# Optimization experiments

Hardware: AMD Instinct MI355X
Metric: run time of the kernel (lower is better)

Reference implementation:

```python
import jax, jax.numpy as jnp
import numpy as np

# --- MLA config (matches init_kwargs) ---
DIM = 2048
H = 16
KV_RANK = 512
Q_RANK = 1536
ROPE = 64          # qk_rope_head_dim (even)
NOPE = 128         # qk_nope_head_dim
VD = 128           # v_head_dim
THETA = 500000.0
EPS = 1e-6
B, T = 1, 2048
QK_HEAD = NOPE + ROPE  # logits use nope + rope dims


def _rmsnorm(x, w):
    # x float32; RMS over last dim, no mean subtraction
    rms = jax.lax.rsqrt(jnp.mean(x * x, axis=-1, keepdims=True) + EPS)
    return (x * rms) * w


def _rope_tables(t):
    inv_freq = 1.0 / (THETA ** (jnp.arange(0, ROPE, 2, dtype=jnp.float32) / ROPE))  # (ROPE/2,)
    pos = jnp.arange(t, dtype=jnp.float32)
    angles = jnp.outer(pos, inv_freq)  # (T, ROPE/2)
    return jnp.cos(angles), jnp.sin(angles)


def _apply_rope(x, cos, sin):
    # x: (B, T, Hx, D) with adjacent-pair rotation; cos/sin: (T, D/2)
    b, t, h, d = x.shape
    xp = x.reshape(b, t, h, d // 2, 2)
    even, odd = xp[..., 0], xp[..., 1]
    c = cos.reshape(1, t, 1, d // 2)
    s = sin.reshape(1, t, 1, d // 2)
    out = jnp.stack((even * c - odd * s, odd * c + even * s), axis=-1)
    return out.reshape(b, t, h, d)


def setup_inputs() -> dict:
    key = jax.random.key(0)
    ks = jax.random.split(key, 7)
    s = 0.02
    x = jax.random.normal(ks[0], (B, T, DIM), dtype=jnp.float32)
    w_q_down = jax.random.normal(ks[1], (Q_RANK, DIM), dtype=jnp.float32) * s
    q_norm_w = jnp.ones((Q_RANK,), dtype=jnp.float32)
    w_q_up = jax.random.normal(ks[2], (H * (NOPE + ROPE), Q_RANK), dtype=jnp.float32) * s
    w_kv_down = jax.random.normal(ks[3], (KV_RANK + ROPE, DIM), dtype=jnp.float32) * s
    kv_norm_w = jnp.ones((KV_RANK,), dtype=jnp.float32)
    w_kv_up = jax.random.normal(ks[4], (H * (NOPE + VD), KV_RANK), dtype=jnp.float32) * s
    w_o = jax.random.normal(ks[5], (DIM, H * VD), dtype=jnp.float32) * s
    return {"x": x, "w_q_down": w_q_down, "q_norm_w": q_norm_w, "w_q_up": w_q_up,
            "w_kv_down": w_kv_down, "kv_norm_w": kv_norm_w, "w_kv_up": w_kv_up, "w_o": w_o}


def reference(x, w_q_down, q_norm_w, w_q_up, w_kv_down, kv_norm_w, w_kv_up, w_o):
    b, t, _ = x.shape
    # Query path: down-proj -> RMSNorm -> up-proj, split nope/rope
    c_q = _rmsnorm(x @ w_q_down.T, q_norm_w)                       # (B,T,Q_RANK)
    q = (c_q @ w_q_up.T).reshape(b, t, H, NOPE + ROPE)
    q_nope, q_rope = q[..., :NOPE], q[..., NOPE:]
    # KV path: down-proj -> split latent c_kv and shared rope key
    kv = x @ w_kv_down.T                                           # (B,T,KV_RANK+ROPE)
    c_kv = kv[..., :KV_RANK]
    k_rope_raw = kv[..., KV_RANK:].reshape(b, t, 1, ROPE)
    # RoPE (adjacent-pair), start_pos=0
    cos, sin = _rope_tables(t)
    q_rope = _apply_rope(q_rope, cos, sin)
    k_rope = _apply_rope(k_rope_raw, cos, sin)                     # (B,T,1,ROPE) shared head
    # Reconstruct k_nope and v from normalized latent
    kv_up = (_rmsnorm(c_kv, kv_norm_w) @ w_kv_up.T).reshape(b, t, H, NOPE + VD)
    k_nope, v = kv_up[..., :NOPE], kv_up[..., NOPE:]
    # Assemble full q/k (rope key broadcast across heads)
    q_full = jnp.concatenate((q_nope, q_rope), axis=-1)            # (B,T,H,QK_HEAD)
    k_full = jnp.concatenate((k_nope, jnp.broadcast_to(k_rope, (b, t, H, ROPE))), axis=-1)
    # Causal attention
    scale = 1.0 / np.sqrt(QK_HEAD)
    scores = jnp.einsum('bqhd,bkhd->bhqk', q_full, k_full) * scale  # (B,H,T,T)
    causal = jnp.tril(jnp.ones((t, t), dtype=bool))
    scores = jnp.where(causal[None, None], scores, -jnp.inf)
    attn = jax.nn.softmax(scores, axis=-1)
    out = jnp.einsum('bhqk,bkhd->bqhd', attn, v).reshape(b, t, H * VD)
    return out @ w_o.T                                             # (B,T,DIM)
```

## Files before the change

kernel.cpp:

```cpp
#include <hip/hip_runtime.h>
#include <hip/hip_bf16.h>

typedef short short8 __attribute__((ext_vector_type(8)));
typedef float f32x4 __attribute__((ext_vector_type(4)));

#define DIM 2048
#define NH 16
#define KV_RANK 512
#define Q_RANK 1536
#define ROPE_D 64
#define NOPE 128
#define VD 128
#define TT 2048
#define QKH 192
#define QD (NH * QKH)
#define KVUP_D (NH * (NOPE + VD))
#define WDN 2176

__device__ inline unsigned short f2bf(float f) {
  __hip_bfloat16 h = __float2bfloat16(f);
  union { __hip_bfloat16 h; unsigned short u; } cv; cv.h = h; return cv.u;
}
__device__ inline float bf2f(unsigned short u) {
  union { unsigned int i; float f; } cv; cv.i = ((unsigned int)u) << 16; return cv.f;
}
__device__ inline void gload_lds16(const void* g, void* l) {
  __builtin_amdgcn_global_load_lds(
      (const __attribute__((address_space(1))) void*)g,
      (__attribute__((address_space(3))) void*)l, 16, 0, 0);
}

__global__ __launch_bounds__(256) void convert_all(
    const float* __restrict__ x, const float* __restrict__ wqd,
    const float* __restrict__ wkvd, const float* __restrict__ wqu,
    const float* __restrict__ wkvu, const float* __restrict__ wo,
    unsigned short* __restrict__ xb, unsigned short* __restrict__ wdb,
    unsigned short* __restrict__ wqub, unsigned short* __restrict__ wkvub,
    unsigned short* __restrict__ wob) {
  int i = blockIdx.x * 256 + threadIdx.x;
  const int n0 = TT * DIM / 4;
  const int n1 = WDN * 2048 / 4;
  const int n2 = QD * Q_RANK / 4;
  const int n3 = KVUP_D * KV_RANK / 4;
  const int n4 = DIM * DIM / 4;
  float4 v;
  unsigned short* dst;
  if (i < n0) { v = reinterpret_cast<const float4*>(x)[i]; dst = xb; }
  else if ((i -= n0) < n1) {
    int row = i >> 9, c4 = i & 511;
    if (row < 1536)      v = reinterpret_cast<const float4*>(wqd)[row * 512 + c4];
    else if (row < 2112) v = reinterpret_cast<const float4*>(wkvd)[(row - 1536) * 512 + c4];
    else                 v = make_float4(0.f, 0.f, 0.f, 0.f);
    dst = wdb;
  }
  else if ((i -= n1) < n2) { v = reinterpret_cast<const float4*>(wqu)[i]; dst = wqub; }
  else if ((i -= n2) < n3) { v = reinterpret_cast<const float4*>(wkvu)[i]; dst = wkvub; }
  else if ((i -= n3) < n4) { v = reinterpret_cast<const float4*>(wo)[i]; dst = wob; }
  else return;
  ushort4 o;
  o.x = f2bf(v.x); o.y = f2bf(v.y); o.z = f2bf(v.z); o.w = f2bf(v.w);
  reinterpret_cast<ushort4*>(dst)[i] = o;
}

__device__ __forceinline__ void gemm_core(const unsigned short* __restrict__ A,
                                          const unsigned short* __restrict__ W,
                                          unsigned short* As, unsigned short* Bs,
                                          int K, int lda, int ldb,
                                          int bm, int bn, int tid,
                                          f32x4 (&acc)[4][4]) {
  const int lane = tid & 63, wave = tid >> 6;
  const int wm = (wave >> 1) * 64, wn = (wave & 1) * 64;
  const int fr = lane & 15, fg = lane >> 4;
  const int sr = lane >> 3, scb = (lane & 7) ^ sr;
  const int r0 = wave * 32;

  const unsigned short* Ag = A + (size_t)(bm + r0 + sr) * lda + scb * 8;
  const unsigned short* Wg = W + (size_t)(bn + r0 + sr) * ldb + scb * 8;
  const int nt = K >> 6;

#pragma unroll
  for (int i = 0; i < 4; ++i) {
    gload_lds16(Ag + (size_t)(i * 8) * lda, As + r0 * 64 + i * 512);
    gload_lds16(Wg + (size_t)(i * 8) * ldb, Bs + r0 * 64 + i * 512);
  }
  int cur = 0;
  for (int t = 0; t < nt; ++t) {
    if (t + 1 < nt) {
      const int nb = cur ^ 1;
      const int ko = (t + 1) * 64;
#pragma unroll
      for (int i = 0; i < 4; ++i) {
        gload_lds16(Ag + ko + (size_t)(i * 8) * lda, As + nb * 8192 + r0 * 64 + i * 512);
        gload_lds16(Wg + ko + (size_t)(i * 8) * ldb, Bs + nb * 8192 + r0 * 64 + i * 512);
      }
      asm volatile("s_waitcnt vmcnt(8)" ::: "memory");
    } else {
      asm volatile("s_waitcnt vmcnt(0)" ::: "memory");
    }
    __builtin_amdgcn_s_barrier();
    asm volatile("" ::: "memory");
    const unsigned short* Ac = As + cur * 8192;
    const unsigned short* Bc = Bs + cur * 8192;
    __builtin_amdgcn_s_setprio(1);
#pragma unroll
    for (int kk = 0; kk < 2; ++kk) {
      short8 a[4], b[4];
#pragma unroll
      for (int i = 0; i < 4; ++i) {
        int ra = wm + i * 16 + fr;
        a[i] = *reinterpret_cast<const short8*>(&Ac[ra * 64 + (((kk * 4 + fg) ^ (ra & 7)) * 8)]);
        int rb = wn + i * 16 + fr;
        b[i] = *reinterpret_cast<const short8*>(&Bc[rb * 64 + (((kk * 4 + fg) ^ (rb & 7)) * 8)]);
      }
#pragma unroll
      for (int i = 0; i < 4; ++i)
#pragma unroll
        for (int j = 0; j < 4; ++j)
          acc[i][j] = __builtin_amdgcn_mfma_f32_16x16x32_bf16(a[i], b[j], acc[i][j], 0, 0, 0);
    }
    __builtin_amdgcn_s_setprio(0);
    asm volatile("" ::: "memory");
    __builtin_amdgcn_s_barrier();
    cur ^= 1;
  }
}

__device__ __forceinline__ void gemm_core_sb(const unsigned short* __restrict__ A,
                                             const unsigned short* __restrict__ W,
                                             unsigned short* As, unsigned short* Bs,
                                             int K, int lda, int ldb,
                                             int bm, int bn, int tid,
                                             f32x4 (&acc)[4][4]) {
  const int lane = tid & 63, wave = tid >> 6;
  const int wm = (wave >> 1) * 64, wn = (wave & 1) * 64;
  const int fr = lane & 15, fg = lane >> 4;
  const int sr = lane >> 3, scb = (lane & 7) ^ sr;
  const int r0 = wave * 32;

  const unsigned short* Ag = A + (size_t)(bm + r0 + sr) * lda + scb * 8;
  const unsigned short* Wg = W + (size_t)(bn + r0 + sr) * ldb + scb * 8;

  for (int k0 = 0; k0 < K; k0 += 64) {
#pragma unroll
    for (int i = 0; i < 4; ++i) {
      gload_lds16(Ag + k0 + (size_t)(i * 8) * lda, As + r0 * 64 + i * 512);
      gload_lds16(Wg + k0 + (size_t)(i * 8) * ldb, Bs + r0 * 64 + i * 512);
    }
    __syncthreads();
    __builtin_amdgcn_s_setprio(1);
#pragma unroll
    for (int kk = 0; kk < 2; ++kk) {
      short8 a[4], b[4];
#pragma unroll
      for (int i = 0; i < 4; ++i) {
        int ra = wm + i * 16 + fr;
        a[i] = *reinterpret_cast<const short8*>(&As[ra * 64 + (((kk * 4 + fg) ^ (ra & 7)) * 8)]);
        int rb = wn + i * 16 + fr;
        b[i] = *reinterpret_cast<const short8*>(&Bs[rb * 64 + (((kk * 4 + fg) ^ (rb & 7)) * 8)]);
      }
#pragma unroll
      for (int i = 0; i < 4; ++i)
#pragma unroll
        for (int j = 0; j < 4; ++j)
          acc[i][j] = __builtin_amdgcn_mfma_f32_16x16x32_bf16(a[i], b[j], acc[i][j], 0, 0, 0);
    }
    __builtin_amdgcn_s_setprio(0);
    __syncthreads();
  }
}

__global__ __launch_bounds__(256) void gemm_fast(const unsigned short* __restrict__ A,
                                                 const unsigned short* __restrict__ W,
                                                 float* __restrict__ Cf,
                                                 unsigned short* __restrict__ Cb,
                                                 int K, int lda, int ldb, int ldc) {
  __shared__ __align__(16) unsigned short As[2 * 128 * 64];
  __shared__ __align__(16) unsigned short Bs[2 * 128 * 64];
  const int tid = threadIdx.x;
  const int bm = blockIdx.y * 128, bn = blockIdx.x * 128;
  const int lane = tid & 63, wave = tid >> 6;
  const int wm = (wave >> 1) * 64, wn = (wave & 1) * 64;
  const int fr = lane & 15, fg = lane >> 4;

  f32x4 acc[4][4] = {};
  gemm_core(A, W, As, Bs, K, lda, ldb, bm, bn, tid, acc);

  if (Cb) {
#pragma unroll
    for (int i = 0; i < 4; ++i) {
      int row0 = bm + wm + i * 16 + fg * 4;
#pragma unroll
      for (int j = 0; j < 4; ++j) {
        int col = bn + wn + j * 16 + fr;
#pragma unroll
        for (int r = 0; r < 4; ++r)
          Cb[(size_t)(row0 + r) * ldc + col] = f2bf(acc[i][j][r]);
      }
    }
  } else {
#pragma unroll
    for (int i = 0; i < 4; ++i) {
      int row0 = bm + wm + i * 16 + fg * 4;
#pragma unroll
      for (int j = 0; j < 4; ++j) {
        int col = bn + wn + j * 16 + fr;
#pragma unroll
        for (int r = 0; r < 4; ++r)
          Cf[(size_t)(row0 + r) * ldc + col] = acc[i][j][r];
      }
    }
  }
}

__global__ __launch_bounds__(256) void gemm_dual(
    const unsigned short* __restrict__ A1, const unsigned short* __restrict__ W1,
    unsigned short* __restrict__ C1,
    const unsigned short* __restrict__ A2, const unsigned short* __restrict__ W2,
    unsigned short* __restrict__ kbuf, unsigned short* __restrict__ vt) {
  __shared__ __align__(16) unsigned short As[128 * 64];
  __shared__ __align__(16) unsigned short Bs[128 * 64];
  const int tid = threadIdx.x;
  const int s = blockIdx.x;
  const unsigned short *A, *W;
  int K, lda, bm, bn;
  const bool isq = (s < 384);
  if (isq) {
    A = A1; W = W1; K = Q_RANK; lda = Q_RANK;
    bn = (s % 24) * 128; bm = (s / 24) * 128;
  } else {
    int b2 = s - 384;
    A = A2; W = W2; K = KV_RANK; lda = KV_RANK;
    bn = (b2 & 31) * 128; bm = (b2 >> 5) * 128;
  }
  const int lane = tid & 63, wave = tid >> 6;
  const int wm = (wave >> 1) * 64, wn = (wave & 1) * 64;
  const int fr = lane & 15, fg = lane >> 4;

  f32x4 acc[4][4] = {};
  gemm_core_sb(A, W, As, Bs, K, lda, lda, bm, bn, tid, acc);

  if (isq) {
#pragma unroll
    for (int i = 0; i < 4; ++i) {
      int row0 = bm + wm + i * 16 + fg * 4;
#pragma unroll
      for (int j = 0; j < 4; ++j) {
        int col = bn + wn + j * 16 + fr;
#pragma unroll
        for (int r = 0; r < 4; ++r)
          C1[(size_t)(row0 + r) * QD + col] = f2bf(acc[i][j][r]);
      }
    }
  } else {
#pragma unroll
    for (int i = 0; i < 4; ++i) {
      int row0 = bm + wm + i * 16 + fg * 4;
#pragma unroll
      for (int j = 0; j < 4; ++j) {
        int col = bn + wn + j * 16 + fr;
        int hh = col >> 8, cc = col & 255;
        if (cc < 128) {
#pragma unroll
          for (int r = 0; r < 4; ++r)
            kbuf[((size_t)hh * TT + row0 + r) * QKH + cc] = f2bf(acc[i][j][r]);
        } else {
          ushort4 w4;
          w4.x = f2bf(acc[i][j][0]); w4.y = f2bf(acc[i][j][1]);
          w4.z = f2bf(acc[i][j][2]); w4.w = f2bf(acc[i][j][3]);
          *reinterpret_cast<ushort4*>(vt + (size_t)(hh * VD + cc - 128) * TT + row0) = w4;
        }
      }
    }
  }
}

__global__ __launch_bounds__(256) void rmsnorm_both(
    const unsigned short* __restrict__ cqkv,
    const float* __restrict__ qw, const float* __restrict__ kvw,
    unsigned short* __restrict__ cq, unsigned short* __restrict__ ckv) {
  const int row = blockIdx.x, tid = threadIdx.x;
  __shared__ float red[256];
  const unsigned short* base = cqkv + (size_t)row * WDN;

#pragma unroll
  for (int ph = 0; ph < 2; ++ph) {
    const int cols = ph ? KV_RANK : Q_RANK;
    const int nch = cols >> 3;
    const unsigned short* x = base + (ph ? Q_RANK : 0);
    const float* w = ph ? kvw : qw;
    unsigned short* out = (ph ? ckv : cq) + (size_t)row * cols;
    float ss = 0.f;
    for (int cb = tid; cb < nch; cb += 256) {
      short8 v = *reinterpret_cast<const short8*>(x + cb * 8);
#pragma unroll
      for (int e = 0; e < 8; ++e) { float f = bf2f((unsigned short)v[e]); ss += f * f; }
    }
    red[tid] = ss; __syncthreads();
    for (int off = 128; off > 0; off >>= 1) {
      if (tid < off) red[tid] += red[tid + off];
      __syncthreads();
    }
    float r = rsqrtf(red[0] / (float)cols + 1e-6f);
    __syncthreads();
    for (int cb = tid; cb < nch; cb += 256) {
      short8 v = *reinterpret_cast<const short8*>(x + cb * 8);
      ushort4 o0, o1;
      o0.x = f2bf(bf2f((unsigned short)v[0]) * r * w[cb * 8 + 0]);
      o0.y = f2bf(bf2f((unsigned short)v[1]) * r * w[cb * 8 + 1]);
      o0.z = f2bf(bf2f((unsigned short)v[2]) * r * w[cb * 8 + 2]);
      o0.w = f2bf(bf2f((unsigned short)v[3]) * r * w[cb * 8 + 3]);
      o1.x = f2bf(bf2f((unsigned short)v[4]) * r * w[cb * 8 + 4]);
      o1.y = f2bf(bf2f((unsigned short)v[5]) * r * w[cb * 8 + 5]);
      o1.z = f2bf(bf2f((unsigned short)v[6]) * r * w[cb * 8 + 6]);
      o1.w = f2bf(bf2f((unsigned short)v[7]) * r * w[cb * 8 + 7]);
      *reinterpret_cast<ushort4*>(out + cb * 8) = o0;
      *reinterpret_cast<ushort4*>(out + cb * 8 + 4) = o1;
    }
  }
}

__global__ __launch_bounds__(256) void rope_kernel(unsigned short* __restrict__ qb,
                                                   const unsigned short* __restrict__ cqkv,
                                                   unsigned short* __restrict__ kbuf) {
  const int t = blockIdx.x, tid = threadIdx.x;
  unsigned short* qrow = qb + (size_t)t * QD;
  for (int p = tid; p < NH * 32 + 32; p += 256) {
    int j = (p < NH * 32) ? (p & 31) : (p - NH * 32);
    float inv = powf(500000.0f, -(float)(2 * j) * (1.0f / 64.0f));
    float ang = (float)t * inv;
    float sv, cv;
    sincosf(ang, &sv, &cv);
    if (p < NH * 32) {
      int h = p >> 5;
      unsigned short* b = qrow + h * QKH + NOPE + 2 * j;
      float e = bf2f(b[0]), o = bf2f(b[1]);
      b[0] = f2bf(e * cv - o * sv);
      b[1] = f2bf(o * cv + e * sv);
    } else {
      const unsigned short* b = cqkv + (size_t)t * WDN + 2048 + 2 * j;
      float e = bf2f(b[0]), o = bf2f(b[1]);
      unsigned short re = f2bf(e * cv - o * sv);
      unsigned short ro = f2bf(o * cv + e * sv);
#pragma unroll
      for (int hh = 0; hh < NH; ++hh) {
        kbuf[((size_t)hh * TT + t) * QKH + NOPE + 2 * j]     = re;
        kbuf[((size_t)hh * TT + t) * QKH + NOPE + 2 * j + 1] = ro;
      }
    }
  }
}

__global__ __launch_bounds__(256, 2) void attn_part(
    const unsigned short* __restrict__ qb,
    const unsigned short* __restrict__ kbuf,
    const unsigned short* __restrict__ vtb,
    unsigned short* __restrict__ Opart,
    float* __restrict__ ml)
{
  const int b = blockIdx.x;
  const int h = b & 15;
  const int w = b >> 4;
  int qt, c;
  if (w < 16)      { qt = 15 - (w >> 2); c = w & 3; }
  else if (w < 28) { int v = w - 16; qt = 11 - v / 3; c = v % 3; }
  else if (w < 36) { qt = 7 - ((w - 28) >> 1); c = (w - 28) & 1; }
  else             { qt = 3 - (w - 36); c = 0; }
  const int t0 = qt * 128;
  const int ktlo = c * 8;
  const int kthi = min(c * 8 + 8, 2 * qt + 2);
  const int tid = threadIdx.x;
  const int lane = tid & 63, wv = tid >> 6;
  const int fr = lane & 15, fg = lane >> 4;

  __shared__ __align__(16) unsigned short KVl[2560 * 8];
  __shared__ __align__(16) unsigned short Ps[4][2][16 * 64];
  unsigned short* Kl = KVl;
  unsigned short* Vt = KVl + 12288;

  short8 qf[2][6];
#pragma unroll
  for (int s = 0; s < 2; ++s) {
    const unsigned short* qrow = qb + (size_t)(t0 + wv * 32 + s * 16 + fr) * QD + h * QKH;
#pragma unroll
    for (int kc = 0; kc < 6; ++kc)
      qf[s][kc] = *reinterpret_cast<const short8*>(qrow + kc * 32 + fg * 8);
  }

  f32x4 o[2][8] = {};
  float m2[2] = {-1e30f, -1e30f};
  float l2[2] = {0.f, 0.f};
  const float scale = 0.0721687836487032f;
  const unsigned short* kb = kbuf + (size_t)h * TT * QKH;
  const unsigned short* vb = vtb + (size_t)h * VD * TT;

  for (int kt = ktlo; kt < kthi; ++kt) {
    const int kt0 = kt * 64;
#pragma unroll
    for (int i = 0; i < 6; ++i) {
      int u = tid + i * 256;
      int row = u / 24, cb = u - (u / 24) * 24;
      int cbs = cb ^ (row & 7);
      gload_lds16(kb + (size_t)(kt0 + row) * QKH + cbs * 8, Kl + u * 8);
    }
#pragma unroll
    for (int i = 0; i < 4; ++i) {
      int u = tid + i * 256;
      int d = u >> 3, cb = u & 7;
      int cbs = cb ^ (d & 7);
      gload_lds16(vb + (size_t)d * TT + kt0 + cbs * 8, Vt + u * 8);
    }
    asm volatile("s_waitcnt vmcnt(0)" ::: "memory");
    __syncthreads();

    f32x4 sA[2][4] = {};
    __builtin_amdgcn_s_setprio(1);
#pragma unroll
    for (int kc = 0; kc < 6; ++kc) {
#pragma unroll
      for (int kr = 0; kr < 4; ++kr) {
        int row = kr * 16 + fr;
        short8 kf = *reinterpret_cast<const short8*>(
            &Kl[row * QKH + (((kc * 4 + fg) ^ (row & 7)) * 8)]);
        sA[0][kr] = __builtin_amdgcn_mfma_f32_16x16x32_bf16(kf, qf[0][kc], sA[0][kr], 0, 0, 0);
        sA[1][kr] = __builtin_amdgcn_mfma_f32_16x16x32_bf16(kf, qf[1][kc], sA[1][kr], 0, 0, 0);
      }
    }
    __builtin_amdgcn_s_setprio(0);

    const bool diag = (kt0 + 64 > t0);
#pragma unroll
    for (int s = 0; s < 2; ++s) {
      const int qg = t0 + wv * 32 + s * 16 + fr;
      float mx = -1e30f;
#pragma unroll
      for (int kr = 0; kr < 4; ++kr)
#pragma unroll
        for (int r = 0; r < 4; ++r) {
          float svv = sA[s][kr][r] * scale;
          if (diag && (kt0 + kr * 16 + fg * 4 + r) > qg) svv = -1e30f;
          sA[s][kr][r] = svv;
          mx = fmaxf(mx, svv);
        }
      mx = fmaxf(mx, __shfl_xor(mx, 16));
      mx = fmaxf(mx, __shfl_xor(mx, 32));
      float mn = fmaxf(m2[s], mx);
      float corr = __expf(m2[s] - mn);
      m2[s] = mn;
      float ssum = 0.f;
#pragma unroll
      for (int kr = 0; kr < 4; ++kr) {
        ushort4 pk;
        float p0 = __expf(sA[s][kr][0] - mn);
        float p1 = __expf(sA[s][kr][1] - mn);
        float p2 = __expf(sA[s][kr][2] - mn);
        float p3 = __expf(sA[s][kr][3] - mn);
        ssum += p0 + p1 + p2 + p3;
        pk.x = f2bf(p0); pk.y = f2bf(p1); pk.z = f2bf(p2); pk.w = f2bf(p3);
        *reinterpret_cast<ushort4*>(
            &Ps[wv][s][fr * 64 + (((kr * 2 + (fg >> 1)) ^ (fr & 7)) * 8) + (fg & 1) * 4]) = pk;
      }
      ssum += __shfl_xor(ssum, 16);
      ssum += __shfl_xor(ssum, 32);
      l2[s] = l2[s] * corr + ssum;
      if (__any(corr != 1.0f)) {
        float c0 = __shfl(corr, fg * 4 + 0);
        float c1 = __shfl(corr, fg * 4 + 1);
        float c2 = __shfl(corr, fg * 4 + 2);
        float c3 = __shfl(corr, fg * 4 + 3);
#pragma unroll
        for (int dj = 0; dj < 8; ++dj) {
          o[s][dj][0] *= c0; o[s][dj][1] *= c1;
          o[s][dj][2] *= c2; o[s][dj][3] *= c3;
        }
      }
    }

    __builtin_amdgcn_s_setprio(1);
#pragma unroll
    for (int kk = 0; kk < 2; ++kk) {
      short8 pa0 = *reinterpret_cast<const short8*>(
          &Ps[wv][0][fr * 64 + (((kk * 4 + fg) ^ (fr & 7)) * 8)]);
      short8 pa1 = *reinterpret_cast<const short8*>(
          &Ps[wv][1][fr * 64 + (((kk * 4 + fg) ^ (fr & 7)) * 8)]);
#pragma unroll
      for (int dj = 0; dj < 8; ++dj) {
        int dv = dj * 16 + fr;
        short8 bv = *reinterpret_cast<const short8*>(
            &Vt[dv * 64 + (((kk * 4 + fg) ^ (dv & 7)) * 8)]);
        o[0][dj] = __builtin_amdgcn_mfma_f32_16x16x32_bf16(pa0, bv, o[0][dj], 0, 0, 0);
        o[1][dj] = __builtin_amdgcn_mfma_f32_16x16x32_bf16(pa1, bv, o[1][dj], 0, 0, 0);
      }
    }
    __builtin_amdgcn_s_setprio(0);
    __syncthreads();
  }

  const int slot = (h * 16 + qt) * 4 + c;
#pragma unroll
  for (int s = 0; s < 2; ++s) {
#pragma unroll
    for (int r = 0; r < 4; ++r) {
      int row = wv * 32 + s * 16 + fg * 4 + r;
      unsigned short* orow = Opart + ((size_t)slot * 128 + row) * 128;
#pragma unroll
      for (int dj = 0; dj < 8; ++dj)
        orow[dj * 16 + fr] = f2bf(o[s][dj][r]);
    }
    if (fg == 0) {
      int row = wv * 32 + s * 16 + fr;
      ml[((size_t)slot * 128 + row) * 2]     = m2[s];
      ml[((size_t)slot * 128 + row) * 2 + 1] = l2[s];
    }
  }
}

__global__ __launch_bounds__(256) void attn_combine(
    const unsigned short* __restrict__ Opart, const float* __restrict__ ml,
    unsigned short* __restrict__ out) {
  const int bid = blockIdx.x;
  const int h = bid >> 5;
  const int qt = (bid >> 1) & 15;
  const int rh = bid & 1;
  const int nch = qt / 4 + 1;
  const int tid = threadIdx.x;
  const int row = rh * 64 + (tid >> 2), dg = tid & 3;
  const int base = (h * 16 + qt) * 4;
  float mm[4], ll[4];
  float M = -1e30f;
#pragma unroll
  for (int cc = 0; cc < 4; ++cc) {
    if (cc < nch) {
      mm[cc] = ml[((size_t)(base + cc) * 128 + row) * 2];
      ll[cc] = ml[((size_t)(base + cc) * 128 + row) * 2 + 1];
      M = fmaxf(M, mm[cc]);
    } else { mm[cc] = -1e30f; ll[cc] = 0.f; }
  }
  float L = 0.f;
#pragma unroll
  for (int cc = 0; cc < 4; ++cc) {
    mm[cc] = __expf(mm[cc] - M);
    L += ll[cc] * mm[cc];
  }
  float acc[32] = {};
#pragma unroll
  for (int cc = 0; cc < 4; ++cc) {
    if (cc < nch) {
      const unsigned short* op = Opart + ((size_t)(base + cc) * 128 + row) * 128 + dg * 32;
      float sc = mm[cc];
#pragma unroll
      for (int e8 = 0; e8 < 4; ++e8) {
        short8 v = *reinterpret_cast<const short8*>(op + e8 * 8);
#pragma unroll
        for (int e = 0; e < 8; ++e) acc[e8 * 8 + e] += bf2f((unsigned short)v[e]) * sc;
      }
    }
  }
  float linv = 1.0f / L;
  unsigned short* dst = out + (size_t)(qt * 128 + row) * DIM + h * VD + dg * 32;
#pragma unroll
  for (int e4 = 0; e4 < 8; ++e4) {
    ushort4 w4;
    w4.x = f2bf(acc[e4 * 4 + 0] * linv);
    w4.y = f2bf(acc[e4 * 4 + 1] * linv);
    w4.z = f2bf(acc[e4 * 4 + 2] * linv);
    w4.w = f2bf(acc[e4 * 4 + 3] * linv);
    *reinterpret_cast<ushort4*>(dst + e4 * 4) = w4;
  }
}

extern "C" void kernel_launch(void* const* d_in, const int* in_sizes, int n_in,
                              void* d_out, int out_size, void* d_ws, size_t ws_size,
                              hipStream_t stream) {
  const float* x        = (const float*)d_in[0];
  const float* w_q_down = (const float*)d_in[1];
  const float* q_norm_w = (const float*)d_in[2];
  const float* w_q_up   = (const float*)d_in[3];
  const float* w_kv_down= (const float*)d_in[4];
  const float* kv_norm_w= (const float*)d_in[5];
  const float* w_kv_up  = (const float*)d_in[6];
  const float* w_o      = (const float*)d_in[7];
  float* outp = (float*)d_out;

  char* ws = (char*)d_ws;
  size_t off = 0;
  auto alloc = [&](size_t bytes) {
    void* p = ws + off;
    off += (bytes + 255) & ~(size_t)255;
    return p;
  };
  unsigned short* x_bf     = (unsigned short*)alloc((size_t)TT * DIM * 2);
  unsigned short* wdown_bf = (unsigned short*)alloc((size_t)WDN * DIM * 2);
  unsigned short* wqu_bf   = (unsigned short*)alloc((size_t)QD * Q_RANK * 2);
  unsigned short* wkvu_bf  = (unsigned short*)alloc((size_t)KVUP_D * KV_RANK * 2);
  unsigned short* wo_bf    = (unsigned short*)alloc((size_t)DIM * DIM * 2);
  unsigned short* cqkv_bf  = (unsigned short*)alloc((size_t)TT * WDN * 2);
  unsigned short* cq_bf    = (unsigned short*)alloc((size_t)TT * Q_RANK * 2);
  unsigned short* ckv_bf   = (unsigned short*)alloc((size_t)TT * KV_RANK * 2);
  unsigned short* qb_bf    = (unsigned short*)alloc((size_t)TT * QD * 2);
  unsigned short* kbuf     = (unsigned short*)alloc((size_t)NH * TT * QKH * 2);
  unsigned short* vtb      = (unsigned short*)alloc((size_t)NH * VD * TT * 2);
  unsigned short* Opart    = (unsigned short*)alloc((size_t)1024 * 128 * 128 * 2);
  float*          mlbuf    = (float*)alloc((size_t)1024 * 128 * 2 * 4);
  unsigned short* attn_bf  = x_bf;

  {
    int total = TT * DIM / 4 + WDN * 2048 / 4 + QD * Q_RANK / 4 +
                KVUP_D * KV_RANK / 4 + DIM * DIM / 4;
    convert_all<<<dim3((total + 255) / 256), dim3(256), 0, stream>>>(
        x, w_q_down, w_kv_down, w_q_up, w_kv_up, w_o,
        x_bf, wdown_bf, wqu_bf, wkvu_bf, wo_bf);
  }

  dim3 blk(256);
  gemm_fast<<<dim3(WDN / 128, TT / 128), blk, 0, stream>>>(
      x_bf, wdown_bf, nullptr, cqkv_bf, DIM, DIM, DIM, WDN);
  rmsnorm_both<<<dim3(TT), blk, 0, stream>>>(cqkv_bf, q_norm_w, kv_norm_w, cq_bf, ckv_bf);
  gemm_dual<<<dim3(896), blk, 0, stream>>>(cq_bf, wqu_bf, qb_bf,
                                           ckv_bf, wkvu_bf, kbuf, vtb);
  rope_kernel<<<dim3(TT), blk, 0, stream>>>(qb_bf, cqkv_bf, kbuf);
  attn_part<<<dim3(640), blk, 0, stream>>>(qb_bf, kbuf, vtb, Opart, mlbuf);
  attn_combine<<<dim3(512), blk, 0, stream>>>(Opart, mlbuf, attn_bf);
  gemm_fast<<<dim3(DIM / 128, TT / 128), blk, 0, stream>>>(
      attn_bf, wo_bf, outp, nullptr, DIM, DIM, DIM, DIM);
}
```

Baseline: 213.1 us.

## Use 64-row GEMM tiles and split attention K/V waits across phases

Replaces the double-buffered 128x128 GEMM with a single-buffered 64x128 tile kernel, doubling the block count for the down-projection and output-projection GEMMs so more CUs are busy. In the attention kernel, the full vmcnt(0) wait before QK^T becomes a partial wait (vmcnt(4)), so the V tile load keeps streaming during score computation and is only waited on before the PV MFMAs. The cost is more A/W reloads per output element and no prefetch overlap in the GEMM.

```diff
diff --git a/kernel.cpp b/kernel.cpp
--- a/kernel.cpp
+++ b/kernel.cpp
@@ -62,69 +62,6 @@
   reinterpret_cast<ushort4*>(dst)[i] = o;
 }
 
-__device__ __forceinline__ void gemm_core(const unsigned short* __restrict__ A,
-                                          const unsigned short* __restrict__ W,
-                                          unsigned short* As, unsigned short* Bs,
-                                          int K, int lda, int ldb,
-                                          int bm, int bn, int tid,
-                                          f32x4 (&acc)[4][4]) {
-  const int lane = tid & 63, wave = tid >> 6;
-  const int wm = (wave >> 1) * 64, wn = (wave & 1) * 64;
-  const int fr = lane & 15, fg = lane >> 4;
-  const int sr = lane >> 3, scb = (lane & 7) ^ sr;
-  const int r0 = wave * 32;
-
-  const unsigned short* Ag = A + (size_t)(bm + r0 + sr) * lda + scb * 8;
-  const unsigned short* Wg = W + (size_t)(bn + r0 + sr) * ldb + scb * 8;
-  const int nt = K >> 6;
-
-#pragma unroll
-  for (int i = 0; i < 4; ++i) {
-    gload_lds16(Ag + (size_t)(i * 8) * lda, As + r0 * 64 + i * 512);
-    gload_lds16(Wg + (size_t)(i * 8) * ldb, Bs + r0 * 64 + i * 512);
-  }
-  int cur = 0;
-  for (int t = 0; t < nt; ++t) {
-    if (t + 1 < nt) {
-      const int nb = cur ^ 1;
-      const int ko = (t + 1) * 64;
-#pragma unroll
-      for (int i = 0; i < 4; ++i) {
-        gload_lds16(Ag + ko + (size_t)(i * 8) * lda, As + nb * 8192 + r0 * 64 + i * 512);
-        gload_lds16(Wg + ko + (size_t)(i * 8) * ldb, Bs + nb * 8192 + r0 * 64 + i * 512);
-      }
-      asm volatile("s_waitcnt vmcnt(8)" ::: "memory");
-    } else {
-      asm volatile("s_waitcnt vmcnt(0)" ::: "memory");
-    }
-    __builtin_amdgcn_s_barrier();
-    asm volatile("" ::: "memory");
-    const unsigned short* Ac = As + cur * 8192;
-    const unsigned short* Bc = Bs + cur * 8192;
-    __builtin_amdgcn_s_setprio(1);
-#pragma unroll
-    for (int kk = 0; kk < 2; ++kk) {
-      short8 a[4], b[4];
-#pragma unroll
-      for (int i = 0; i < 4; ++i) {
-        int ra = wm + i * 16 + fr;
-        a[i] = *reinterpret_cast<const short8*>(&Ac[ra * 64 + (((kk * 4 + fg) ^ (ra & 7)) * 8)]);
-        int rb = wn + i * 16 + fr;
-        b[i] = *reinterpret_cast<const short8*>(&Bc[rb * 64 + (((kk * 4 + fg) ^ (rb & 7)) * 8)]);
-      }
-#pragma unroll
-      for (int i = 0; i < 4; ++i)
-#pragma unroll
-        for (int j = 0; j < 4; ++j)
-          acc[i][j] = __builtin_amdgcn_mfma_f32_16x16x32_bf16(a[i], b[j], acc[i][j], 0, 0, 0);
-    }
-    __builtin_amdgcn_s_setprio(0);
-    asm volatile("" ::: "memory");
-    __builtin_amdgcn_s_barrier();
-    cur ^= 1;
-  }
-}
-
 __device__ __forceinline__ void gemm_core_sb(const unsigned short* __restrict__ A,
                                              const unsigned short* __restrict__ W,
                                              unsigned short* As, unsigned short* Bs,
@@ -169,25 +106,62 @@
   }
 }
 
-__global__ __launch_bounds__(256) void gemm_fast(const unsigned short* __restrict__ A,
-                                                 const unsigned short* __restrict__ W,
-                                                 float* __restrict__ Cf,
-                                                 unsigned short* __restrict__ Cb,
-                                                 int K, int lda, int ldb, int ldc) {
-  __shared__ __align__(16) unsigned short As[2 * 128 * 64];
-  __shared__ __align__(16) unsigned short Bs[2 * 128 * 64];
+__global__ __launch_bounds__(256) void gemm_m64(const unsigned short* __restrict__ A,
+                                                const unsigned short* __restrict__ W,
+                                                float* __restrict__ Cf,
+                                                unsigned short* __restrict__ Cb,
+                                                int K, int lda, int ldb, int ldc) {
+  __shared__ __align__(16) unsigned short As[64 * 64];
+  __shared__ __align__(16) unsigned short Bs[128 * 64];
   const int tid = threadIdx.x;
-  const int bm = blockIdx.y * 128, bn = blockIdx.x * 128;
+  const int bm = blockIdx.y * 64, bn = blockIdx.x * 128;
   const int lane = tid & 63, wave = tid >> 6;
-  const int wm = (wave >> 1) * 64, wn = (wave & 1) * 64;
+  const int wm = (wave >> 1) * 32, wn = (wave & 1) * 64;
   const int fr = lane & 15, fg = lane >> 4;
 
-  f32x4 acc[4][4] = {};
-  gemm_core(A, W, As, Bs, K, lda, ldb, bm, bn, tid, acc);
+  f32x4 acc[2][4] = {};
+
+  for (int k0 = 0; k0 < K; k0 += 64) {
+#pragma unroll
+    for (int i = 0; i < 2; ++i) {
+      int u = tid + i * 256;
+      int row = u >> 3, cb = u & 7;
+      gload_lds16(A + (size_t)(bm + row) * lda + k0 + ((cb ^ (row & 7)) * 8), As + u * 8);
+    }
+#pragma unroll
+    for (int i = 0; i < 4; ++i) {
+      int u = tid + i * 256;
+      int row = u >> 3, cb = u & 7;
+      gload_lds16(W + (size_t)(bn + row) * ldb + k0 + ((cb ^ (row & 7)) * 8), Bs + u * 8);
+    }
+    __syncthreads();
+    __builtin_amdgcn_s_setprio(1);
+#pragma unroll
+    for (int kk = 0; kk < 2; ++kk) {
+      short8 a[2], b[4];
+#pragma unroll
+      for (int i = 0; i < 2; ++i) {
+        int ra = wm + i * 16 + fr;
+        a[i] = *reinterpret_cast<const short8*>(&As[ra * 64 + (((kk * 4 + fg) ^ (ra & 7)) * 8)]);
+      }
+#pragma unroll
+      for (int j = 0; j < 4; ++j) {
+        int rb = wn + j * 16 + fr;
+        b[j] = *reinterpret_cast<const short8*>(&Bs[rb * 64 + (((kk * 4 + fg) ^ (rb & 7)) * 8)]);
+      }
+#pragma unroll
+      for (int i = 0; i < 2; ++i)
+#pragma unroll
+        for (int j = 0; j < 4; ++j)
+          acc[i][j] = __builtin_amdgcn_mfma_f32_16x16x32_bf16(a[i], b[j], acc[i][j], 0, 0, 0);
+    }
+    __builtin_amdgcn_s_setprio(0);
+    __syncthreads();
+  }
 
   if (Cb) {
 #pragma unroll
-    for (int i = 0; i < 4; ++i) {
+    for (int i = 0; i < 2; ++i) {
       int row0 = bm + wm + i * 16 + fg * 4;
 #pragma unroll
       for (int j = 0; j < 4; ++j) {
@@ -199,7 +173,7 @@
     }
   } else {
 #pragma unroll
-    for (int i = 0; i < 4; ++i) {
+    for (int i = 0; i < 2; ++i) {
       int row0 = bm + wm + i * 16 + fg * 4;
 #pragma unroll
       for (int j = 0; j < 4; ++j) {
@@ -385,6 +359,7 @@
     for (int kc = 0; kc < 6; ++kc)
       qf[s][kc] = *reinterpret_cast<const short8*>(qrow + kc * 32 + fg * 8);
   }
+  asm volatile("s_waitcnt vmcnt(0)" ::: "memory");
 
   f32x4 o[2][8] = {};
   float m2[2] = {-1e30f, -1e30f};
@@ -409,8 +384,9 @@
       int cbs = cb ^ (d & 7);
       gload_lds16(vb + (size_t)d * TT + kt0 + cbs * 8, Vt + u * 8);
     }
-    asm volatile("s_waitcnt vmcnt(0)" ::: "memory");
-    __syncthreads();
+    asm volatile("s_waitcnt vmcnt(4)" ::: "memory");
+    __builtin_amdgcn_s_barrier();
+    asm volatile("" ::: "memory");
 
     f32x4 sA[2][4] = {};
     __builtin_amdgcn_s_setprio(1);
@@ -475,6 +451,10 @@
       }
     }
 
+    asm volatile("s_waitcnt vmcnt(0)" ::: "memory");
+    __builtin_amdgcn_s_barrier();
+    asm volatile("" ::: "memory");
+
     __builtin_amdgcn_s_setprio(1);
 #pragma unroll
     for (int kk = 0; kk < 2; ++kk) {
@@ -492,7 +472,8 @@
       }
     }
     __builtin_amdgcn_s_setprio(0);
-    __syncthreads();
+    asm volatile("" ::: "memory");
+    __builtin_amdgcn_s_barrier();
   }
 
   const int slot = (h * 16 + qt) * 4 + c;
@@ -612,7 +593,7 @@
   }
 
   dim3 blk(256);
-  gemm_fast<<<dim3(WDN / 128, TT / 128), blk, 0, stream>>>(
+  gemm_m64<<<dim3(WDN / 128, TT / 64), blk, 0, stream>>>(
       x_bf, wdown_bf, nullptr, cqkv_bf, DIM, DIM, DIM, WDN);
   rmsnorm_both<<<dim3(TT), blk, 0, stream>>>(cqkv_bf, q_norm_w, kv_norm_w, cq_bf, ckv_bf);
   gemm_dual<<<dim3(896), blk, 0, stream>>>(cq_bf, wqu_bf, qb_bf,
@@ -620,6 +601,6 @@
   rope_kernel<<<dim3(TT), blk, 0, stream>>>(qb_bf, cqkv_bf, kbuf);
   attn_part<<<dim3(640), blk, 0, stream>>>(qb_bf, kbuf, vtb, Opart, mlbuf);
   attn_combine<<<dim3(512), blk, 0, stream>>>(Opart, mlbuf, attn_bf);
-  gemm_fast<<<dim3(DIM / 128, TT / 128), blk, 0, stream>>>(
+  gemm_m64<<<dim3(DIM / 128, TT / 64), blk, 0, stream>>>(
       attn_bf, wo_bf, outp, nullptr, DIM, DIM, DIM, DIM);
 }
```

New measurement: 205.6 us (median of 2 runs). 1.04x faster.
